# Performance work log

Hardware: AMD Instinct MI355X
Metric: run time of the kernel (lower is better)

Reference implementation:

```python
import jax, jax.numpy as jnp
import numpy as np
from jax import lax

B, T, H, W, E = 64, 8, 8, 8, 512
REC = 2048


def setup_inputs() -> dict:
    key = jax.random.key(0)
    kx, kwi, kwr = jax.random.split(key, 3)
    x = jax.random.normal(kx, (B, T, H, W, E), dtype=jnp.float32)
    W_input = jax.random.normal(kwi, (E, REC), dtype=jnp.float32) / np.sqrt(E)
    W_recurrent = jax.random.normal(kwr, (REC, REC), dtype=jnp.float32) / np.sqrt(REC)
    return {"x": x, "W_input": W_input, "W_recurrent": W_recurrent}


def reference(x, W_input, W_recurrent):
    b, t, h, w, e = x.shape
    R = t * h * w
    rec = W_recurrent.shape[0]
    k = int(rec * 0.4)  # 819, matches torch: int(recurrent_size * 0.4)
    x_seq = jnp.swapaxes(x.reshape(b, R, e), 0, 1)  # [R, B, E]
    row_idx = jnp.arange(b)[:, None]

    def step(r, inp):
        z = r @ W_recurrent                    # [B, REC]
        vals, idx = lax.top_k(z, k)            # [B, k]
        s = jnp.zeros_like(z).at[row_idx, idx].set(vals)  # scatter top-k back
        r_new = jnp.tanh(inp @ W_input + s)
        r_new = r_new / (jnp.linalg.norm(r_new, axis=-1, keepdims=True) + 1e-6)
        return r_new, None

    r0 = jnp.zeros((b, rec), dtype=x.dtype)
    r_final, _ = lax.scan(step, r0, x_seq)
    return r_final
```

## Files before the change

kernel.cpp:

```cpp
#include <hip/hip_runtime.h>

#define NSTEP 512
#define EDIM  512
#define REC   2048
#define NB    64
#define KSEL  819
#define KC    8
#define ZCH   256
#define AP    264
#define CSTR  16896

typedef unsigned short u16;
typedef __bf16 bf16x8 __attribute__((ext_vector_type(8)));
typedef float  f32x4  __attribute__((ext_vector_type(4)));
typedef unsigned long long ull;

static __device__ __forceinline__ f32x4 mfma16(bf16x8 a, bf16x8 b, f32x4 c) {
    return __builtin_amdgcn_mfma_f32_16x16x32_bf16(a, b, c, 0, 0, 0);
}

static __device__ __forceinline__ void split2(float v, u16& c0, u16& c1) {
    __bf16 b0 = (__bf16)v;
    __bf16 b1 = (__bf16)(v - (float)b0);
    c0 = __builtin_bit_cast(u16, b0);
    c1 = __builtin_bit_cast(u16, b1);
}

static __device__ __forceinline__ void cstore4f(float* p, float v) {
    __hip_atomic_store((unsigned*)p, __float_as_uint(v), __ATOMIC_RELAXED, __HIP_MEMORY_SCOPE_AGENT);
}
static __device__ __forceinline__ void cstore4u(unsigned* p, unsigned v) {
    __hip_atomic_store(p, v, __ATOMIC_RELAXED, __HIP_MEMORY_SCOPE_AGENT);
}
static __device__ __forceinline__ unsigned cload4u(const unsigned* p) {
    return __hip_atomic_load(p, __ATOMIC_RELAXED, __HIP_MEMORY_SCOPE_AGENT);
}
static __device__ __forceinline__ void cstore8u(void* p, ull v) {
    __hip_atomic_store((ull*)p, v, __ATOMIC_RELAXED, __HIP_MEMORY_SCOPE_AGENT);
}
static __device__ __forceinline__ ull cload8u(const void* p) {
    return __hip_atomic_load((const ull*)p, __ATOMIC_RELAXED, __HIP_MEMORY_SCOPE_AGENT);
}
static __device__ __forceinline__ float2 cload8f(const float* p) {
    ull u = cload8u(p);
    float2 v; __builtin_memcpy(&v, &u, 8);
    return v;
}

__device__ __forceinline__ void gbarA(unsigned* bar, int bid, int tid,
                                      unsigned gen, bool wait)
{
    __syncthreads();
    if (tid == 0) cstore4u(&bar[bid], gen);
    if (bid == 0 && tid < 64) {
        const ull* sl = (const ull*)bar;
        for (;;) {
            const ull v0 = cload8u(&sl[tid * 2]);
            const ull v1 = cload8u(&sl[tid * 2 + 1]);
            const bool ok = ((unsigned)v0 >= gen) && ((unsigned)(v0 >> 32) >= gen)
                         && ((unsigned)v1 >= gen) && ((unsigned)(v1 >> 32) >= gen);
            if (__all(ok)) break;
            __builtin_amdgcn_s_sleep(1);
        }
        if (tid < 16) cstore4u(&bar[1024 + tid * 32], gen);
    }
    if (wait) {
        if (tid == 0) {
            const int g = bid >> 4;
            while (cload4u(&bar[1024 + g * 32]) < gen)
                __builtin_amdgcn_s_sleep(1);
            __asm__ volatile("" ::: "memory");
        }
        __syncthreads();
    }
}

__device__ __forceinline__ void gbarB(unsigned* bar, int bid, int tid, unsigned gen)
{
    __syncthreads();
    if (bid < NB && tid == 0) cstore4u(&bar[512 + bid], gen);
    if (bid == 0 && tid < 64) {
        for (;;) {
            const unsigned v = cload4u(&bar[512 + tid]);
            if (__all(v >= gen)) break;
            __builtin_amdgcn_s_sleep(1);
        }
        if (tid < 16) cstore4u(&bar[1536 + tid * 32], gen);
    }
    if (tid == 0) {
        const int g = bid >> 4;
        while (cload4u(&bar[1536 + g * 32]) < gen)
            __builtin_amdgcn_s_sleep(1);
        __asm__ volatile("" ::: "memory");
    }
    __syncthreads();
}

__global__ __launch_bounds__(512, 1)
void rnn_persistent(const float* __restrict__ x, const float* __restrict__ Wi,
                    const float* __restrict__ Wr, float* __restrict__ out,
                    u16* __restrict__ rTu, float* __restrict__ zb,
                    u16* __restrict__ Ybf, unsigned* __restrict__ bar)
{
    extern __shared__ __align__(16) char smem[];
    u16* WrSu = (u16*)smem;
    u16* aSu  = (u16*)(smem + 67584);
    float* WiP = (float*)smem;
    float* xP  = (float*)(smem + 16384);
    unsigned*      kS    = (unsigned*)(smem + 67584);
    unsigned char* selS  = (unsigned char*)(smem + 67584 + 8192);
    unsigned*      hist  = (unsigned*)(smem + 67584 + 10240);
    __shared__ unsigned s_byte, s_newrem, s_cnteq;
    __shared__ float red[8];

    const int bid = blockIdx.x;
    const int tid = threadIdx.x;
    const int kc = bid & 7, nc = bid >> 3;
    const int n0 = nc * 64, kcbase = kc * ZCH;
    const int wid = tid >> 6, lane = tid & 63;
    const int q = lane >> 4, l16 = lane & 15;
    const int Moff = (wid & 3) * 16, Npair = wid >> 2;
    const bool isB = (bid < NB);

    {
        const int t0 = bid * 2;
        const int tr4 = (tid >> 5) * 4;
        const int tc4 = (tid & 31) * 4;
        for (int nc2 = 0; nc2 < 16; ++nc2) {
            const int n0y = nc2 * 128;
            f32x4 acc[2][4];
#pragma unroll
            for (int h = 0; h < 2; ++h)
#pragma unroll
                for (int i = 0; i < 4; ++i) acc[h][i] = (f32x4){0,0,0,0};
            for (int kr = 0; kr < 16; ++kr) {
                const int k0y = kr * 32;
                __syncthreads();
                {
                    const int col4 = (tid & 31) * 4, row = tid >> 5;
                    *(float4*)&WiP[row * 128 + col4] =
                        *(const float4*)(Wi + (long long)(k0y + row) * REC + n0y + col4);
                    *(float4*)&WiP[(row + 16) * 128 + col4] =
                        *(const float4*)(Wi + (long long)(k0y + row + 16) * REC + n0y + col4);
                }
                for (int h = 0; h < 2; ++h) {
                    __syncthreads();
                    {
                        const int b = tid & 63, e4 = (tid >> 6) * 4;
                        const float4 v = *(const float4*)(x + ((long long)b * NSTEP + (t0 + h)) * EDIM + k0y + e4);
                        xP[(e4    ) * 64 + b] = v.x;
                        xP[(e4 + 1) * 64 + b] = v.y;
                        xP[(e4 + 2) * 64 + b] = v.z;
                        xP[(e4 + 3) * 64 + b] = v.w;
                    }
                    __syncthreads();
#pragma unroll 8
                    for (int kk = 0; kk < 32; ++kk) {
                        const float4 af = *(const float4*)&xP[kk * 64 + tr4];
                        const float4 bf = *(const float4*)&WiP[kk * 128 + tc4];
                        const float av[4] = {af.x, af.y, af.z, af.w};
#pragma unroll
                        for (int i = 0; i < 4; ++i) {
                            acc[h][i].x += av[i] * bf.x;
                            acc[h][i].y += av[i] * bf.y;
                            acc[h][i].z += av[i] * bf.z;
                            acc[h][i].w += av[i] * bf.w;
                        }
                    }
                }
            }
#pragma unroll
            for (int h = 0; h < 2; ++h)
#pragma unroll
                for (int i = 0; i < 4; ++i) {
                    const long long yrow = (long long)(t0 + h) * 64 + tr4 + i;
                    u16 o[4];
                    o[0] = __builtin_bit_cast(u16, (__bf16)acc[h][i].x);
                    o[1] = __builtin_bit_cast(u16, (__bf16)acc[h][i].y);
                    o[2] = __builtin_bit_cast(u16, (__bf16)acc[h][i].z);
                    o[3] = __builtin_bit_cast(u16, (__bf16)acc[h][i].w);
                    ull pk; __builtin_memcpy(&pk, o, 8);
                    cstore8u(&Ybf[yrow * REC + n0y + tc4], pk);
                }
        }
    }
    {
        const int g = bid * 512 + tid;
        if (g < 65536) cstore8u(rTu + (long long)g * 4, 0ull);
        cstore4f(zb + g, 0.f);
    }
    gbarA(bar, bid, tid, 1u, true);

    {
        for (int it = 0; it < 32; ++it) {
            const int row = it * 8 + wid;
            const int col = lane;
            const float v = Wr[(long long)(kcbase + row) * REC + n0 + col];
            u16 s0, s1; split2(v, s0, s1);
            const int base = col * AP + row;
            WrSu[base] = s0;
            WrSu[CSTR + base] = s1;
        }
        __syncthreads();
    }

    const int hw = tid >> 5, hl = tid & 31;
    for (int t = 0; t < NSTEP; ++t) {
        float* zcur = zb + (size_t)(t & 1) * 131072;
        float* znxt = zb + (size_t)((t + 1) & 1) * 131072;
        cstore4f(znxt + bid * 512 + tid, 0.f);
        {
            ull va[8], vbv[8];
#pragma unroll
            for (int i = 0; i < 8; ++i) {
                const int c = i >> 2;
                const int b = (i & 3) * 16 + hw;
                const u16* src = rTu + (long long)c * 131072 + (long long)b * REC + kcbase + hl * 8;
                va[i] = cload8u(src);
                vbv[i] = cload8u(src + 4);
            }
#pragma unroll
            for (int i = 0; i < 8; ++i) {
                const int c = i >> 2;
                const int b = (i & 3) * 16 + hw;
                u16* dst = aSu + c * CSTR + b * AP + hl * 8;
                *(ull*)dst = va[i];
                *(ull*)(dst + 4) = vbv[i];
            }
        }
        __syncthreads();

        f32x4 acc0 = {0,0,0,0}, acc1 = {0,0,0,0};
#pragma unroll
        for (int ks = 0; ks < 8; ++ks) {
            const int kk = ks * 32 + q * 8;
            const u16* ap = aSu + (Moff + l16) * AP + kk;
            bf16x8 A0 = *(const bf16x8*)(ap);
            bf16x8 A1 = *(const bf16x8*)(ap + CSTR);
            const u16* bp0 = WrSu + (Npair * 32 + l16) * AP + kk;
            bf16x8 B00 = *(const bf16x8*)(bp0);
            bf16x8 B01 = *(const bf16x8*)(bp0 + CSTR);
            const u16* bp1 = bp0 + 16 * AP;
            bf16x8 B10 = *(const bf16x8*)(bp1);
            bf16x8 B11 = *(const bf16x8*)(bp1 + CSTR);
            acc0 = mfma16(A0, B00, acc0);
            acc1 = mfma16(A0, B10, acc1);
            acc0 = mfma16(A0, B01, acc0);
            acc1 = mfma16(A0, B11, acc1);
            acc0 = mfma16(A1, B00, acc0);
            acc1 = mfma16(A1, B10, acc1);
        }
        {
            const int colA = n0 + Npair * 32 + l16;
#pragma unroll
            for (int i = 0; i < 4; ++i) {
                float* zp = zcur + (long long)(Moff + q * 4 + i) * REC + colA;
                unsafeAtomicAdd(zp,      ((float*)&acc0)[i]);
                unsafeAtomicAdd(zp + 16, ((float*)&acc1)[i]);
            }
        }
        gbarA(bar, bid, tid, (unsigned)(t + 2), isB);

        if (isB) {
            const int b = bid;
            const int j0 = tid * 4;
            float zs[4];
            {
                const float2 u0 = cload8f(zcur + (long long)b * REC + j0);
                const float2 u1 = cload8f(zcur + (long long)b * REC + j0 + 2);
                zs[0] = u0.x; zs[1] = u0.y; zs[2] = u1.x; zs[3] = u1.y;
            }
            const ushort4 yv = *(const ushort4*)&Ybf[((long long)t * 64 + b) * REC + j0];
            unsigned kv[4];
#pragma unroll
            for (int s = 0; s < 4; ++s) {
                const unsigned u = __float_as_uint(zs[s]);
                kv[s] = (u & 0x80000000u) ? ~u : (u | 0x80000000u);
            }
            unsigned* hw_ = hist + wid * 256;
            unsigned prefix = 0, remaining = KSEL;
            int done = 0;
            for (int byte = 3; byte >= 0 && !done; --byte) {
                {
                    uint4 zz = {0u, 0u, 0u, 0u};
                    *(uint4*)&hw_[lane * 4] = zz;
                }
                const int shift = byte * 8;
                const unsigned pmask = (byte == 3) ? 0u : (0xFFFFFFFFu << (shift + 8));
#pragma unroll
                for (int s = 0; s < 4; ++s) {
                    if ((kv[s] & pmask) == prefix)
                        atomicAdd(&hw_[(kv[s] >> shift) & 255u], 1u);
                }
                __syncthreads();
                if (tid < 64) {
                    unsigned c0 = 0, c1 = 0, c2 = 0, c3 = 0;
#pragma unroll
                    for (int w = 0; w < 8; ++w) {
                        const uint4 hv = *(const uint4*)&hist[w * 256 + tid * 4];
                        c0 += hv.x; c1 += hv.y; c2 += hv.z; c3 += hv.w;
                    }
                    const unsigned tot = c0 + c1 + c2 + c3;
                    unsigned suf = tot;
#pragma unroll
                    for (int st = 1; st < 64; st <<= 1) {
                        unsigned o = __shfl_down(suf, (unsigned)st);
                        if (tid + st >= 64) o = 0u;
                        suf += o;
                    }
                    unsigned S[5];
                    S[0] = suf; S[1] = suf - c0; S[2] = suf - c0 - c1;
                    S[3] = suf - c0 - c1 - c2; S[4] = suf - tot;
                    const unsigned cc[4] = {c0, c1, c2, c3};
#pragma unroll
                    for (int qq = 0; qq < 4; ++qq) {
                        if (S[qq] >= remaining && S[qq + 1] < remaining) {
                            s_byte = (unsigned)(tid * 4 + qq);
                            s_newrem = remaining - S[qq + 1];
                            s_cnteq = cc[qq];
                        }
                    }
                }
                __syncthreads();
                prefix |= (s_byte << shift);
                remaining = s_newrem;
                if (remaining == s_cnteq) done = 1;
            }
            unsigned char sel[4];
            if (done) {
#pragma unroll
                for (int s = 0; s < 4; ++s)
                    sel[s] = (kv[s] >= prefix) ? 1 : 0;
            } else {
                *(uint4*)&kS[j0] = *(uint4*)kv;
                __syncthreads();
                if (tid == 0) {
                    unsigned rem = remaining;
                    const unsigned T = prefix;
                    for (int j = 0; j < REC; ++j) {
                        const unsigned k = kS[j];
                        unsigned char sl = 0;
                        if (k > T) sl = 1;
                        else if (k == T && rem > 0u) { sl = 1; --rem; }
                        selS[j] = sl;
                    }
                }
                __syncthreads();
#pragma unroll
                for (int s = 0; s < 4; ++s) sel[s] = selS[j0 + s];
            }
            float rn[4]; float ss = 0.f;
            const u16 ya[4] = {yv.x, yv.y, yv.z, yv.w};
#pragma unroll
            for (int s = 0; s < 4; ++s) {
                const float y = __uint_as_float(((unsigned)ya[s]) << 16);
                const float v = y + (sel[s] ? zs[s] : 0.f);
                const float th = tanhf(v);
                rn[s] = th; ss += th * th;
            }
#pragma unroll
            for (int off = 32; off > 0; off >>= 1)
                ss += __shfl_down(ss, (unsigned)off);
            if (lane == 0) red[wid] = ss;
            __syncthreads();
            float a = 0.f;
#pragma unroll
            for (int i = 0; i < 8; ++i) a += red[i];
            const float inv = 1.0f / (sqrtf(a) + 1e-6f);
            u16 o0[4], o1[4];
            float4 ov;
#pragma unroll
            for (int s = 0; s < 4; ++s) {
                const float v = rn[s] * inv;
                split2(v, o0[s], o1[s]);
                ((float*)&ov)[s] = v;
            }
            ull p0, p1;
            __builtin_memcpy(&p0, o0, 8); __builtin_memcpy(&p1, o1, 8);
            cstore8u(rTu + (long long)b * REC + j0, p0);
            cstore8u(rTu + 131072 + (long long)b * REC + j0, p1);
            if (t == NSTEP - 1)
                *(float4*)&out[(long long)b * REC + j0] = ov;
        }
        gbarB(bar, bid, tid, (unsigned)(t + 1));
    }
}

extern "C" void kernel_launch(void* const* d_in, const int* in_sizes, int n_in,
                              void* d_out, int out_size, void* d_ws, size_t ws_size,
                              hipStream_t stream)
{
    const float* x   = (const float*)d_in[0];
    const float* Win = (const float*)d_in[1];
    const float* Wr  = (const float*)d_in[2];
    float* out = (float*)d_out;

    char* ws = (char*)d_ws;
    const size_t BAR = 8192;
    unsigned* bar = (unsigned*)ws;
    float* zb  = (float*)(ws + BAR);
    u16*   rTu = (u16*)(ws + BAR + 2 * 524288);
    u16*   Ybf = (u16*)(ws + BAR + 2 * 524288 + 524288);

    static int smem_set = 0;
    if (!smem_set) {
        hipFuncSetAttribute((const void*)rnn_persistent,
                            hipFuncAttributeMaxDynamicSharedMemorySize, 135168);
        smem_set = 1;
    }
    hipMemsetAsync(bar, 0, BAR, stream);
    rnn_persistent<<<256, 512, 135168, stream>>>(x, Win, Wr, out, rTu, zb, Ybf, bar);
}
```

Baseline: 7.594 ms.

## Replace atomic z reduction with per-chunk partials and flat spin barriers

Each K-chunk block now writes its partial z tile to its own buffer with plain stores, and the 64 batch-owner blocks sum the 8 partials themselves. This removes the float atomics and the zeroing of the next z buffer. The two-level hierarchical barriers become direct flag polling: owners wait on all 256 flags, and every block waits on the 64 owner flags. Owners also store unnormalised tanh outputs in fp32 plus a per-row inverse norm, so the bf16 split and normalisation move into the consumers' A-tile load. The trade is more global reads per owner and much wider flag polling.

```diff
diff --git a/kernel.cpp b/kernel.cpp
--- a/kernel.cpp
+++ b/kernel.cpp
@@ -29,6 +29,9 @@
 static __device__ __forceinline__ void cstore4f(float* p, float v) {
     __hip_atomic_store((unsigned*)p, __float_as_uint(v), __ATOMIC_RELAXED, __HIP_MEMORY_SCOPE_AGENT);
 }
+static __device__ __forceinline__ float cload4f(const float* p) {
+    return __uint_as_float(__hip_atomic_load((const unsigned*)p, __ATOMIC_RELAXED, __HIP_MEMORY_SCOPE_AGENT));
+}
 static __device__ __forceinline__ void cstore4u(unsigned* p, unsigned v) {
     __hip_atomic_store(p, v, __ATOMIC_RELAXED, __HIP_MEMORY_SCOPE_AGENT);
 }
@@ -46,61 +49,18 @@
     float2 v; __builtin_memcpy(&v, &u, 8);
     return v;
 }
-
-__device__ __forceinline__ void gbarA(unsigned* bar, int bid, int tid,
-                                      unsigned gen, bool wait)
-{
-    __syncthreads();
-    if (tid == 0) cstore4u(&bar[bid], gen);
-    if (bid == 0 && tid < 64) {
-        const ull* sl = (const ull*)bar;
-        for (;;) {
-            const ull v0 = cload8u(&sl[tid * 2]);
-            const ull v1 = cload8u(&sl[tid * 2 + 1]);
-            const bool ok = ((unsigned)v0 >= gen) && ((unsigned)(v0 >> 32) >= gen)
-                         && ((unsigned)v1 >= gen) && ((unsigned)(v1 >> 32) >= gen);
-            if (__all(ok)) break;
-            __builtin_amdgcn_s_sleep(1);
-        }
-        if (tid < 16) cstore4u(&bar[1024 + tid * 32], gen);
-    }
-    if (wait) {
-        if (tid == 0) {
-            const int g = bid >> 4;
-            while (cload4u(&bar[1024 + g * 32]) < gen)
-                __builtin_amdgcn_s_sleep(1);
-            __asm__ volatile("" ::: "memory");
-        }
-        __syncthreads();
-    }
-}
-
-__device__ __forceinline__ void gbarB(unsigned* bar, int bid, int tid, unsigned gen)
-{
-    __syncthreads();
-    if (bid < NB && tid == 0) cstore4u(&bar[512 + bid], gen);
-    if (bid == 0 && tid < 64) {
-        for (;;) {
-            const unsigned v = cload4u(&bar[512 + tid]);
-            if (__all(v >= gen)) break;
-            __builtin_amdgcn_s_sleep(1);
-        }
-        if (tid < 16) cstore4u(&bar[1536 + tid * 32], gen);
-    }
-    if (tid == 0) {
-        const int g = bid >> 4;
-        while (cload4u(&bar[1536 + g * 32]) < gen)
-            __builtin_amdgcn_s_sleep(1);
-        __asm__ volatile("" ::: "memory");
-    }
-    __syncthreads();
+static __device__ __forceinline__ void cstore8f(float* p, float a, float b) {
+    float2 v; v.x = a; v.y = b;
+    ull u; __builtin_memcpy(&u, &v, 8);
+    cstore8u(p, u);
 }
 
 __global__ __launch_bounds__(512, 1)
 void rnn_persistent(const float* __restrict__ x, const float* __restrict__ Wi,
                     const float* __restrict__ Wr, float* __restrict__ out,
-                    u16* __restrict__ rTu, float* __restrict__ zb,
-                    u16* __restrict__ Ybf, unsigned* __restrict__ bar)
+                    float* __restrict__ rTf, float* __restrict__ invb,
+                    float* __restrict__ zpart, u16* __restrict__ Ybf,
+                    unsigned* __restrict__ bar)
 {
     extern __shared__ __align__(16) char smem[];
     u16* WrSu = (u16*)smem;
@@ -112,6 +72,7 @@
     unsigned*      hist  = (unsigned*)(smem + 67584 + 10240);
     __shared__ unsigned s_byte, s_newrem, s_cnteq;
     __shared__ float red[8];
+    __shared__ float invS[64];
 
     const int bid = blockIdx.x;
     const int tid = threadIdx.x;
@@ -186,10 +147,14 @@
     }
     {
         const int g = bid * 512 + tid;
-        if (g < 65536) cstore8u(rTu + (long long)g * 4, 0ull);
-        cstore4f(zb + g, 0.f);
-    }
-    gbarA(bar, bid, tid, 1u, true);
+        cstore4f(rTf + g, 0.f);
+        if (bid == 0 && tid < 64) cstore4f(invb + tid, 0.f);
+    }
+    __syncthreads();
+    if (tid == 0) cstore4u(&bar[bid], 1u);
+    if (tid < 256) { while (cload4u(&bar[tid]) < 1u) __builtin_amdgcn_s_sleep(1); }
+    __asm__ volatile("" ::: "memory");
+    __syncthreads();
 
     {
         for (int it = 0; it < 32; ++it) {
@@ -204,28 +169,26 @@
         __syncthreads();
     }
 
-    const int hw = tid >> 5, hl = tid & 31;
     for (int t = 0; t < NSTEP; ++t) {
-        float* zcur = zb + (size_t)(t & 1) * 131072;
-        float* znxt = zb + (size_t)((t + 1) & 1) * 131072;
-        cstore4f(znxt + bid * 512 + tid, 0.f);
         {
-            ull va[8], vbv[8];
-#pragma unroll
-            for (int i = 0; i < 8; ++i) {
-                const int c = i >> 2;
-                const int b = (i & 3) * 16 + hw;
-                const u16* src = rTu + (long long)c * 131072 + (long long)b * REC + kcbase + hl * 8;
-                va[i] = cload8u(src);
-                vbv[i] = cload8u(src + 4);
-            }
-#pragma unroll
-            for (int i = 0; i < 8; ++i) {
-                const int c = i >> 2;
-                const int b = (i & 3) * 16 + hw;
-                u16* dst = aSu + c * CSTR + b * AP + hl * 8;
-                *(ull*)dst = va[i];
-                *(ull*)(dst + 4) = vbv[i];
+            if (tid < 64) invS[tid] = cload4f(invb + tid);
+            float2 v[16];
+#pragma unroll
+            for (int i = 0; i < 16; ++i) {
+                const int f = i * 512 + tid;
+                v[i] = cload8f(rTf + (f >> 7) * REC + kcbase + (f & 127) * 2);
+            }
+            __syncthreads();
+#pragma unroll
+            for (int i = 0; i < 16; ++i) {
+                const int f = i * 512 + tid;
+                const int b = f >> 7, k = (f & 127) * 2;
+                const float iv = invS[b];
+                u16 x0c0, x0c1, x1c0, x1c1;
+                split2(v[i].x * iv, x0c0, x0c1);
+                split2(v[i].y * iv, x1c0, x1c1);
+                *(unsigned*)&aSu[b * AP + k]        = (unsigned)x0c0 | ((unsigned)x1c0 << 16);
+                *(unsigned*)&aSu[CSTR + b * AP + k] = (unsigned)x0c1 | ((unsigned)x1c1 << 16);
             }
         }
         __syncthreads();
@@ -252,25 +215,36 @@
         }
         {
             const int colA = n0 + Npair * 32 + l16;
+            float* zp = zpart + kc * 131072;
 #pragma unroll
             for (int i = 0; i < 4; ++i) {
-                float* zp = zcur + (long long)(Moff + q * 4 + i) * REC + colA;
-                unsafeAtomicAdd(zp,      ((float*)&acc0)[i]);
-                unsafeAtomicAdd(zp + 16, ((float*)&acc1)[i]);
-            }
-        }
-        gbarA(bar, bid, tid, (unsigned)(t + 2), isB);
+                float* p = zp + (Moff + q * 4 + i) * REC + colA;
+                cstore4f(p,      ((float*)&acc0)[i]);
+                cstore4f(p + 16, ((float*)&acc1)[i]);
+            }
+        }
+
+        __syncthreads();
+        if (tid == 0) cstore4u(&bar[bid], (unsigned)(t + 2));
 
         if (isB) {
             const int b = bid;
             const int j0 = tid * 4;
-            float zs[4];
-            {
-                const float2 u0 = cload8f(zcur + (long long)b * REC + j0);
-                const float2 u1 = cload8f(zcur + (long long)b * REC + j0 + 2);
-                zs[0] = u0.x; zs[1] = u0.y; zs[2] = u1.x; zs[3] = u1.y;
-            }
             const ushort4 yv = *(const ushort4*)&Ybf[((long long)t * 64 + b) * REC + j0];
+            if (tid < 256) {
+                while (cload4u(&bar[tid]) < (unsigned)(t + 2)) __builtin_amdgcn_s_sleep(1);
+            }
+            __asm__ volatile("" ::: "memory");
+            __syncthreads();
+
+            float zs[4] = {0.f, 0.f, 0.f, 0.f};
+#pragma unroll
+            for (int c = 0; c < 8; ++c) {
+                const float* zp = zpart + c * 131072 + b * REC + j0;
+                const float2 u0 = cload8f(zp);
+                const float2 u1 = cload8f(zp + 2);
+                zs[0] += u0.x; zs[1] += u0.y; zs[2] += u1.x; zs[3] += u1.y;
+            }
             unsigned kv[4];
 #pragma unroll
             for (int s = 0; s < 4; ++s) {
@@ -349,15 +323,17 @@
 #pragma unroll
                 for (int s = 0; s < 4; ++s) sel[s] = selS[j0 + s];
             }
-            float rn[4]; float ss = 0.f;
+            float th4[4]; float ss = 0.f;
             const u16 ya[4] = {yv.x, yv.y, yv.z, yv.w};
 #pragma unroll
             for (int s = 0; s < 4; ++s) {
                 const float y = __uint_as_float(((unsigned)ya[s]) << 16);
-                const float v = y + (sel[s] ? zs[s] : 0.f);
-                const float th = tanhf(v);
-                rn[s] = th; ss += th * th;
-            }
+                const float vv = y + (sel[s] ? zs[s] : 0.f);
+                const float th = tanhf(vv);
+                th4[s] = th; ss += th * th;
+            }
+            cstore8f(rTf + b * REC + j0,     th4[0], th4[1]);
+            cstore8f(rTf + b * REC + j0 + 2, th4[2], th4[3]);
 #pragma unroll
             for (int off = 32; off > 0; off >>= 1)
                 ss += __shfl_down(ss, (unsigned)off);
@@ -367,22 +343,22 @@
 #pragma unroll
             for (int i = 0; i < 8; ++i) a += red[i];
             const float inv = 1.0f / (sqrtf(a) + 1e-6f);
-            u16 o0[4], o1[4];
-            float4 ov;
-#pragma unroll
-            for (int s = 0; s < 4; ++s) {
-                const float v = rn[s] * inv;
-                split2(v, o0[s], o1[s]);
-                ((float*)&ov)[s] = v;
-            }
-            ull p0, p1;
-            __builtin_memcpy(&p0, o0, 8); __builtin_memcpy(&p1, o1, 8);
-            cstore8u(rTu + (long long)b * REC + j0, p0);
-            cstore8u(rTu + 131072 + (long long)b * REC + j0, p1);
-            if (t == NSTEP - 1)
+            if (tid == 0) cstore4f(invb + b, inv);
+            if (t == NSTEP - 1) {
+                float4 ov;
+                ov.x = th4[0] * inv; ov.y = th4[1] * inv;
+                ov.z = th4[2] * inv; ov.w = th4[3] * inv;
                 *(float4*)&out[(long long)b * REC + j0] = ov;
-        }
-        gbarB(bar, bid, tid, (unsigned)(t + 1));
+            }
+        }
+
+        __syncthreads();
+        if (isB && tid == 0) cstore4u(&bar[512 + bid], (unsigned)(t + 1));
+        if (tid < 64) {
+            while (cload4u(&bar[512 + tid]) < (unsigned)(t + 1)) __builtin_amdgcn_s_sleep(1);
+        }
+        __asm__ volatile("" ::: "memory");
+        __syncthreads();
     }
 }
 
@@ -397,10 +373,11 @@
 
     char* ws = (char*)d_ws;
     const size_t BAR = 8192;
-    unsigned* bar = (unsigned*)ws;
-    float* zb  = (float*)(ws + BAR);
-    u16*   rTu = (u16*)(ws + BAR + 2 * 524288);
-    u16*   Ybf = (u16*)(ws + BAR + 2 * 524288 + 524288);
+    unsigned* bar  = (unsigned*)ws;
+    float*    invb = (float*)(ws + 4096);
+    float*    zpart = (float*)(ws + BAR);
+    float*    rTf  = (float*)(ws + BAR + 4194304);
+    u16*      Ybf  = (u16*)(ws + BAR + 4194304 + 524288);
 
     static int smem_set = 0;
     if (!smem_set) {
@@ -409,5 +386,5 @@
         smem_set = 1;
     }
     hipMemsetAsync(bar, 0, BAR, stream);
-    rnn_persistent<<<256, 512, 135168, stream>>>(x, Win, Wr, out, rTu, zb, Ybf, bar);
-}
+    rnn_persistent<<<256, 512, 135168, stream>>>(x, Win, Wr, out, rTf, invb, zpart, Ybf, bar);
+}
```

Result: slower. 9.782 ms (+28.8%).
